# Kernel optimization log

Hardware: AMD Instinct MI355X
Metric: run time of the kernel (lower is better)

Reference implementation:

```python
import jax, jax.numpy as jnp
import numpy as np

N = 100000
C = 64
E = 3200000
NUM_LAYERS = 10
ALPHA = 0.9


def setup_inputs() -> dict:
    key = jax.random.key(0)
    k1, k2, k3, k4 = jax.random.split(key, 4)
    labels = jax.random.uniform(k1, (N, C), dtype=jnp.float32)
    mask = jax.random.randint(k2, (N,), 0, 2).astype(jnp.bool_)
    src = jax.random.randint(k3, (E,), 0, N, dtype=jnp.int32)
    dst = jax.random.randint(k4, (E,), 0, N, dtype=jnp.int32)
    return {"labels": labels, "mask": mask, "src": src, "dst": dst}


def reference(labels, mask, src, dst):
    # in-degrees: number of incoming edges per node, clamped to >= 1
    degs = jax.ops.segment_sum(jnp.ones((E,), dtype=jnp.float32), dst,
                               num_segments=N)
    degs = jnp.maximum(degs, 1.0)
    norm = (degs ** -0.5)[:, None]  # [N, 1]

    # seed only the masked (known) labels
    y = jnp.where(mask[:, None], labels, 0.0)
    last = (1.0 - ALPHA) * y

    def step(y, _):
        h = (y * norm)[src]                                   # gather  [E, C]
        agg = jax.ops.segment_sum(h, dst, num_segments=N)     # scatter [N, C]
        y = jnp.clip(last + ALPHA * agg * norm, 0.0, 1.0)     # post_step clamp
        return y, None

    y, _ = jax.lax.scan(step, y, None, length=NUM_LAYERS)
    return y
```

## Files before the change

### kernel.cpp

```cpp
#include <hip/hip_runtime.h>
#include <hip/hip_fp16.h>

#define N_LAYERS 10
#define ALPHA_F 0.9f
#define CAP 80
#define NRANGES 8

__global__ void detect_mask_kernel(const unsigned char* __restrict__ m,
                                   int* __restrict__ flag, int nbytes) {
    __shared__ int cnt;
    if (threadIdx.x == 0) cnt = 0;
    __syncthreads();
    int c = 0;
    for (int i = threadIdx.x; i < nbytes; i += blockDim.x) {
        if ((i & 3) != 0 && m[i] != 0) c++;
    }
    atomicAdd(&cnt, c);
    __syncthreads();
    if (threadIdx.x == 0) *flag = (cnt > 0) ? 1 : 0;
}

__global__ __launch_bounds__(256) void fillcap_kernel(
    const int* __restrict__ src, const int* __restrict__ dst,
    int* __restrict__ cnt, int* __restrict__ csr,
    int N, int E, int M, int range) {
    int r = blockIdx.x & (NRANGES - 1);
    int m = blockIdx.x >> 3;
    int rlo = r * range;
    int rhi = rlo + range; if (rhi > N) rhi = N;
    unsigned urlo = (unsigned)rlo;
    unsigned urng = (unsigned)(rhi - rlo);
    int stride = M * 256;
    int nv = E >> 2;
    const int4* s4p = (const int4*)src;
    const int4* d4p = (const int4*)dst;
    for (int i = m * 256 + threadIdx.x; i < nv; i += stride) {
        int4 d4 = d4p[i];
        int4 s4 = s4p[i];
        bool v0 = ((unsigned)d4.x - urlo) < urng;
        bool v1 = ((unsigned)d4.y - urlo) < urng;
        bool v2 = ((unsigned)d4.z - urlo) < urng;
        bool v3 = ((unsigned)d4.w - urlo) < urng;
        int p0 = v0 ? atomicAdd(cnt + d4.x, 1) : CAP;
        int p1 = v1 ? atomicAdd(cnt + d4.y, 1) : CAP;
        int p2 = v2 ? atomicAdd(cnt + d4.z, 1) : CAP;
        int p3 = v3 ? atomicAdd(cnt + d4.w, 1) : CAP;
        if (p0 < CAP) csr[(size_t)d4.x * CAP + p0] = s4.x;
        if (p1 < CAP) csr[(size_t)d4.y * CAP + p1] = s4.y;
        if (p2 < CAP) csr[(size_t)d4.z * CAP + p2] = s4.z;
        if (p3 < CAP) csr[(size_t)d4.w * CAP + p3] = s4.w;
    }
    if (m == 0) {
        for (int i = (nv << 2) + threadIdx.x; i < E; i += 256) {
            int d = dst[i];
            if (((unsigned)d - urlo) < urng) {
                int p = atomicAdd(cnt + d, 1);
                if (p < CAP) csr[(size_t)d * CAP + p] = src[i];
            }
        }
    }
}

__global__ void norm_kernel(const int* __restrict__ cnt,
                            float* __restrict__ norm, int N) {
    int i = blockIdx.x * blockDim.x + threadIdx.x;
    if (i < N) {
        int d = cnt[i];
        norm[i] = rsqrtf((float)(d > 0 ? d : 1));
    }
}

__global__ __launch_bounds__(256) void degree_kernel(
    const int* __restrict__ dst, int* __restrict__ cursor,
    int N, int E, int M, int range) {
    int r = blockIdx.x & (NRANGES - 1);
    int m = blockIdx.x >> 3;
    int rlo = r * range;
    int rhi = rlo + range; if (rhi > N) rhi = N;
    int stride = M * 256;
    for (int i = m * 256 + threadIdx.x; i < E; i += stride) {
        int d = dst[i];
        if (d >= rlo && d < rhi) atomicAdd(&cursor[d], 1);
    }
}

__global__ __launch_bounds__(256) void scan_blocks_kernel(
    const int* __restrict__ deg, int* __restrict__ local,
    int* __restrict__ btot, int N) {
    __shared__ int tmp[256];
    int i = blockIdx.x * 256 + threadIdx.x;
    int d = (i < N) ? deg[i] : 0;
    tmp[threadIdx.x] = d;
    __syncthreads();
    for (int off = 1; off < 256; off <<= 1) {
        int v = (threadIdx.x >= off) ? tmp[threadIdx.x - off] : 0;
        __syncthreads();
        tmp[threadIdx.x] += v;
        __syncthreads();
    }
    if (i < N) local[i] = tmp[threadIdx.x] - d;
    if (threadIdx.x == 255) btot[blockIdx.x] = tmp[255];
}

__global__ __launch_bounds__(512) void scan_tops_kernel(int* __restrict__ btot,
                                                        int nb) {
    __shared__ int tmp[512];
    int d = (threadIdx.x < nb) ? btot[threadIdx.x] : 0;
    tmp[threadIdx.x] = d;
    __syncthreads();
    for (int off = 1; off < 512; off <<= 1) {
        int v = (threadIdx.x >= off) ? tmp[threadIdx.x - off] : 0;
        __syncthreads();
        tmp[threadIdx.x] += v;
        __syncthreads();
    }
    if (threadIdx.x < nb) btot[threadIdx.x] = tmp[threadIdx.x] - d;
}

__global__ __launch_bounds__(256) void scan_apply_kernel(
    const int* __restrict__ local, const int* __restrict__ btot,
    int* __restrict__ cursor, int* __restrict__ offsets,
    float* __restrict__ norm, int N, int E) {
    int i = blockIdx.x * 256 + threadIdx.x;
    if (i >= N) return;
    int d = cursor[i];
    int off = local[i] + btot[blockIdx.x];
    offsets[i] = off;
    cursor[i] = off;
    norm[i] = rsqrtf((float)(d > 0 ? d : 1));
    if (i == N - 1) offsets[N] = E;
}

__global__ __launch_bounds__(256) void fill_kernel(
    const int* __restrict__ src, const int* __restrict__ dst,
    int* __restrict__ cursor, int* __restrict__ csr,
    int N, int E, int M, int range) {
    int r = blockIdx.x & (NRANGES - 1);
    int m = blockIdx.x >> 3;
    int rlo = r * range;
    int rhi = rlo + range; if (rhi > N) rhi = N;
    int stride = M * 256;
    for (int i = m * 256 + threadIdx.x; i < E; i += stride) {
        int d = dst[i];
        if (d >= rlo && d < rhi) {
            int pos = atomicAdd(&cursor[d], 1);
            csr[pos] = src[i];
        }
    }
}

__global__ void init_kernel(const float* __restrict__ labels,
                            const void* __restrict__ mask,
                            const int* __restrict__ flag,
                            const float* __restrict__ norm,
                            __half* __restrict__ y0,
                            __half* __restrict__ last_h, int NC) {
    int idx = blockIdx.x * blockDim.x + threadIdx.x;
    if (idx >= NC) return;
    int n = idx >> 6;
    bool m = (*flag) ? (((const unsigned char*)mask)[n] != 0)
                     : (((const int*)mask)[n] != 0);
    float ym = m ? labels[idx] : 0.0f;
    y0[idx] = __float2half(ym * norm[n]);
    last_h[idx] = __float2half(0.1f * ym);
}

__global__ __launch_bounds__(256) void prop_kernel(
    const int* __restrict__ degc, const int* __restrict__ offsets,
    const int* __restrict__ csr, const float* __restrict__ norm,
    const __half* __restrict__ last_h, const __half* __restrict__ yin,
    __half* __restrict__ yout, float* __restrict__ out_final,
    int N, int use_cap) {
    int wave = threadIdx.x >> 6;
    int lane = threadIdx.x & 63;
    int n = blockIdx.x * 4 + wave;
    if (n >= N) return;

    int deg; size_t base;
    if (use_cap) {
        deg = degc[n]; if (deg > CAP) deg = CAP;
        base = (size_t)n * CAP;
    } else {
        int s = offsets[n];
        deg = offsets[n + 1] - s;
        base = (size_t)s;
    }

    int grp = lane >> 3;
    int sub = lane & 7;
    const float4* yin4 = (const float4*)yin;

    float acc[8];
    #pragma unroll
    for (int k = 0; k < 8; ++k) acc[k] = 0.0f;

    for (int b0 = 0; b0 < deg; b0 += 64) {
        int cb = deg - b0; if (cb > 64) cb = 64;
        int li = lane < cb ? lane : cb - 1;
        int sid = csr[base + b0 + li];
        #pragma unroll
        for (int j = 0; j < 8; ++j) {
            int e = j * 8 + grp;
            int es = e < cb ? e : cb - 1;
            float msk = e < cb ? 1.0f : 0.0f;
            int s = __shfl(sid, es);
            float4 v = yin4[(size_t)s * 8 + sub];
            const __half2* h = (const __half2*)&v;
            float2 f0 = __half22float2(h[0]);
            float2 f1 = __half22float2(h[1]);
            float2 f2 = __half22float2(h[2]);
            float2 f3 = __half22float2(h[3]);
            acc[0] = fmaf(msk, f0.x, acc[0]);
            acc[1] = fmaf(msk, f0.y, acc[1]);
            acc[2] = fmaf(msk, f1.x, acc[2]);
            acc[3] = fmaf(msk, f1.y, acc[3]);
            acc[4] = fmaf(msk, f2.x, acc[4]);
            acc[5] = fmaf(msk, f2.y, acc[5]);
            acc[6] = fmaf(msk, f3.x, acc[6]);
            acc[7] = fmaf(msk, f3.y, acc[7]);
        }
    }

    #pragma unroll
    for (int k = 0; k < 8; ++k) {
        acc[k] += __shfl_xor(acc[k], 8);
        acc[k] += __shfl_xor(acc[k], 16);
        acc[k] += __shfl_xor(acc[k], 32);
    }

    float nrm = norm[n];
    float4 lv = ((const float4*)(last_h + ((size_t)n << 6)))[sub];
    const __half2* lh = (const __half2*)&lv;
    float2 g0 = __half22float2(lh[0]);
    float2 g1 = __half22float2(lh[1]);
    float2 g2 = __half22float2(lh[2]);
    float2 g3 = __half22float2(lh[3]);
    float lastv[8] = {g0.x, g0.y, g1.x, g1.y, g2.x, g2.y, g3.x, g3.y};

    float y[8];
    #pragma unroll
    for (int k = 0; k < 8; ++k) {
        float t = lastv[k] + ALPHA_F * acc[k] * nrm;
        y[k] = fminf(fmaxf(t, 0.0f), 1.0f);
    }

    if (grp == 0) {
        if (out_final) {
            float4* op = (float4*)(out_final + ((size_t)n << 6)) + (sub << 1);
            op[0] = make_float4(y[0], y[1], y[2], y[3]);
            op[1] = make_float4(y[4], y[5], y[6], y[7]);
        } else {
            __half2 h0 = __float22half2_rn(make_float2(y[0] * nrm, y[1] * nrm));
            __half2 h1 = __float22half2_rn(make_float2(y[2] * nrm, y[3] * nrm));
            __half2 h2 = __float22half2_rn(make_float2(y[4] * nrm, y[5] * nrm));
            __half2 h3 = __float22half2_rn(make_float2(y[6] * nrm, y[7] * nrm));
            float4 pack;
            ((__half2*)&pack)[0] = h0;
            ((__half2*)&pack)[1] = h1;
            ((__half2*)&pack)[2] = h2;
            ((__half2*)&pack)[3] = h3;
            ((float4*)(yout + ((size_t)n << 6)))[sub] = pack;
        }
    }
}

extern "C" void kernel_launch(void* const* d_in, const int* in_sizes, int n_in,
                              void* d_out, int out_size, void* d_ws,
                              size_t ws_size, hipStream_t stream) {
    const float* labels = (const float*)d_in[0];
    const void* mask = d_in[1];
    const int* src = (const int*)d_in[2];
    const int* dst = (const int*)d_in[3];
    int NC = in_sizes[0];
    int N = in_sizes[1];
    int E = in_sizes[2];

    char* p = (char*)d_ws;
    size_t used = 0;
    auto carve = [&](size_t bytes) -> char* {
        char* r = p;
        size_t a = (bytes + 255) & ~(size_t)255;
        p += a;
        used += a;
        return r;
    };
    int* flag      = (int*)carve(sizeof(int));
    float* norm    = (float*)carve((size_t)N * sizeof(float));
    int* cnt       = (int*)carve((size_t)(N + 1) * sizeof(int));
    __half* last_h = (__half*)carve((size_t)NC * sizeof(__half));
    __half* bufA   = (__half*)carve((size_t)NC * sizeof(__half));
    __half* bufB   = (__half*)carve((size_t)NC * sizeof(__half));

    size_t cap_need = ((size_t)N * CAP * sizeof(int) + 255) & ~(size_t)255;
    size_t cmp_need = (((size_t)E * sizeof(int) + 255) & ~(size_t)255) +
                      3 * (((size_t)(N + 1) * sizeof(int) + 255) & ~(size_t)255) +
                      1024 * sizeof(int) + 4096;
    bool use_cap = (used + cap_need) <= ws_size;

    int range = (N + NRANGES - 1) / NRANGES;
    int dbytes = N < 4096 ? N : 4096;
    detect_mask_kernel<<<1, 256, 0, stream>>>((const unsigned char*)mask, flag,
                                              dbytes);

    if (use_cap) {
        int* csr = (int*)carve((size_t)N * CAP * sizeof(int));
        hipMemsetAsync(cnt, 0, (size_t)N * sizeof(int), stream);
        int M = 256;
        fillcap_kernel<<<NRANGES * M, 256, 0, stream>>>(src, dst, cnt, csr, N,
                                                        E, M, range);
        norm_kernel<<<(N + 255) / 256, 256, 0, stream>>>(cnt, norm, N);
        init_kernel<<<(NC + 255) / 256, 256, 0, stream>>>(labels, mask, flag,
                                                          norm, bufA, last_h,
                                                          NC);
        __half* bufs[2] = {bufA, bufB};
        for (int l = 0; l < N_LAYERS; ++l) {
            bool fin = (l == N_LAYERS - 1);
            prop_kernel<<<(N + 3) / 4, 256, 0, stream>>>(
                cnt, cnt, csr, norm, last_h, bufs[l & 1], bufs[(l + 1) & 1],
                fin ? (float*)d_out : nullptr, N, 1);
        }
    } else {
        (void)cmp_need;
        int* offsets = (int*)carve((size_t)(N + 1) * sizeof(int));
        int* local   = (int*)carve((size_t)(N + 1) * sizeof(int));
        int* btot    = (int*)carve((size_t)1024 * sizeof(int));
        int* csr     = (int*)carve((size_t)E * sizeof(int));
        hipMemsetAsync(cnt, 0, (size_t)N * sizeof(int), stream);
        int M = 128;
        degree_kernel<<<NRANGES * M, 256, 0, stream>>>(dst, cnt, N, E, M,
                                                       range);
        int nscan = (N + 255) / 256;
        scan_blocks_kernel<<<nscan, 256, 0, stream>>>(cnt, local, btot, N);
        scan_tops_kernel<<<1, 512, 0, stream>>>(btot, nscan);
        scan_apply_kernel<<<nscan, 256, 0, stream>>>(local, btot, cnt, offsets,
                                                     norm, N, E);
        fill_kernel<<<NRANGES * M, 256, 0, stream>>>(src, dst, cnt, csr, N, E,
                                                     M, range);
        init_kernel<<<(NC + 255) / 256, 256, 0, stream>>>(labels, mask, flag,
                                                          norm, bufA, last_h,
                                                          NC);
        __half* bufs[2] = {bufA, bufB};
        for (int l = 0; l < N_LAYERS; ++l) {
            bool fin = (l == N_LAYERS - 1);
            prop_kernel<<<(N + 3) / 4, 256, 0, stream>>>(
                cnt, offsets, csr, norm, last_h, bufs[l & 1],
                bufs[(l + 1) & 1], fin ? (float*)d_out : nullptr, N, 0);
        }
    }
}
```

Measured before the change: 976.3 us.

## Split propagation into two channel-half passes with nontemporal loads and stores

Each layer's propagation now runs as two launches, each covering 32 of the 64 channels. Within a launch, 16 edge groups of 4 lanes gather 64-byte half rows, so the working set of gathered features per pass is halved and should fit better in cache. Nontemporal hints are added for the CSR index loads, the last_h loads and the output stores so they do not evict the gathered feature data. The cost is twice the launches and a second read of the CSR indices per layer.

```diff
diff --git a/kernel.cpp b/kernel.cpp
--- a/kernel.cpp
+++ b/kernel.cpp
@@ -5,6 +5,19 @@
 #define ALPHA_F 0.9f
 #define CAP 80
 #define NRANGES 8
+
+typedef float nfloat4 __attribute__((ext_vector_type(4)));
+
+__device__ __forceinline__ float4 nt_load4(const float4* p) {
+    nfloat4 v = __builtin_nontemporal_load((const nfloat4*)p);
+    float4 r;
+    r.x = v.x; r.y = v.y; r.z = v.z; r.w = v.w;
+    return r;
+}
+__device__ __forceinline__ void nt_store4(float4* p, float4 v) {
+    nfloat4 t = {v.x, v.y, v.z, v.w};
+    __builtin_nontemporal_store(t, (nfloat4*)p);
+}
 
 __global__ void detect_mask_kernel(const unsigned char* __restrict__ m,
                                    int* __restrict__ flag, int nbytes) {
@@ -170,7 +183,7 @@
     const int* __restrict__ csr, const float* __restrict__ norm,
     const __half* __restrict__ last_h, const __half* __restrict__ yin,
     __half* __restrict__ yout, float* __restrict__ out_final,
-    int N, int use_cap) {
+    int N, int use_cap, int half) {
     int wave = threadIdx.x >> 6;
     int lane = threadIdx.x & 63;
     int n = blockIdx.x * 4 + wave;
@@ -186,9 +199,10 @@
         base = (size_t)s;
     }
 
-    int grp = lane >> 3;
-    int sub = lane & 7;
+    int grp = lane >> 2;
+    int sub = lane & 3;
     const float4* yin4 = (const float4*)yin;
+    int hoff = half << 2;
 
     float acc[8];
     #pragma unroll
@@ -197,14 +211,14 @@
     for (int b0 = 0; b0 < deg; b0 += 64) {
         int cb = deg - b0; if (cb > 64) cb = 64;
         int li = lane < cb ? lane : cb - 1;
-        int sid = csr[base + b0 + li];
+        int sid = __builtin_nontemporal_load(csr + base + b0 + li);
         #pragma unroll
-        for (int j = 0; j < 8; ++j) {
-            int e = j * 8 + grp;
+        for (int j = 0; j < 4; ++j) {
+            int e = j * 16 + grp;
             int es = e < cb ? e : cb - 1;
             float msk = e < cb ? 1.0f : 0.0f;
             int s = __shfl(sid, es);
-            float4 v = yin4[(size_t)s * 8 + sub];
+            float4 v = yin4[(size_t)s * 8 + hoff + sub];
             const __half2* h = (const __half2*)&v;
             float2 f0 = __half22float2(h[0]);
             float2 f1 = __half22float2(h[1]);
@@ -223,13 +237,16 @@
 
     #pragma unroll
     for (int k = 0; k < 8; ++k) {
+        acc[k] += __shfl_xor(acc[k], 4);
         acc[k] += __shfl_xor(acc[k], 8);
         acc[k] += __shfl_xor(acc[k], 16);
         acc[k] += __shfl_xor(acc[k], 32);
     }
 
     float nrm = norm[n];
-    float4 lv = ((const float4*)(last_h + ((size_t)n << 6)))[sub];
+    const float4* lptr =
+        (const float4*)(last_h + ((size_t)n << 6) + (half << 5)) + sub;
+    float4 lv = nt_load4(lptr);
     const __half2* lh = (const __half2*)&lv;
     float2 g0 = __half22float2(lh[0]);
     float2 g1 = __half22float2(lh[1]);
@@ -246,9 +263,10 @@
 
     if (grp == 0) {
         if (out_final) {
-            float4* op = (float4*)(out_final + ((size_t)n << 6)) + (sub << 1);
-            op[0] = make_float4(y[0], y[1], y[2], y[3]);
-            op[1] = make_float4(y[4], y[5], y[6], y[7]);
+            float4* op = (float4*)(out_final + ((size_t)n << 6) + (half << 5)) +
+                         (sub << 1);
+            nt_store4(op, make_float4(y[0], y[1], y[2], y[3]));
+            nt_store4(op + 1, make_float4(y[4], y[5], y[6], y[7]));
         } else {
             __half2 h0 = __float22half2_rn(make_float2(y[0] * nrm, y[1] * nrm));
             __half2 h1 = __float22half2_rn(make_float2(y[2] * nrm, y[3] * nrm));
@@ -259,7 +277,9 @@
             ((__half2*)&pack)[1] = h1;
             ((__half2*)&pack)[2] = h2;
             ((__half2*)&pack)[3] = h3;
-            ((float4*)(yout + ((size_t)n << 6)))[sub] = pack;
+            float4* op =
+                (float4*)(yout + ((size_t)n << 6) + (half << 5)) + sub;
+            nt_store4(op, pack);
         }
     }
 }
@@ -292,9 +312,6 @@
     __half* bufB   = (__half*)carve((size_t)NC * sizeof(__half));
 
     size_t cap_need = ((size_t)N * CAP * sizeof(int) + 255) & ~(size_t)255;
-    size_t cmp_need = (((size_t)E * sizeof(int) + 255) & ~(size_t)255) +
-                      3 * (((size_t)(N + 1) * sizeof(int) + 255) & ~(size_t)255) +
-                      1024 * sizeof(int) + 4096;
     bool use_cap = (used + cap_need) <= ws_size;
 
     int range = (N + NRANGES - 1) / NRANGES;
@@ -315,12 +332,13 @@
         __half* bufs[2] = {bufA, bufB};
         for (int l = 0; l < N_LAYERS; ++l) {
             bool fin = (l == N_LAYERS - 1);
-            prop_kernel<<<(N + 3) / 4, 256, 0, stream>>>(
-                cnt, cnt, csr, norm, last_h, bufs[l & 1], bufs[(l + 1) & 1],
-                fin ? (float*)d_out : nullptr, N, 1);
+            for (int h = 0; h < 2; ++h) {
+                prop_kernel<<<(N + 3) / 4, 256, 0, stream>>>(
+                    cnt, cnt, csr, norm, last_h, bufs[l & 1], bufs[(l + 1) & 1],
+                    fin ? (float*)d_out : nullptr, N, 1, h);
+            }
         }
     } else {
-        (void)cmp_need;
         int* offsets = (int*)carve((size_t)(N + 1) * sizeof(int));
         int* local   = (int*)carve((size_t)(N + 1) * sizeof(int));
         int* btot    = (int*)carve((size_t)1024 * sizeof(int));
@@ -342,9 +360,11 @@
         __half* bufs[2] = {bufA, bufB};
         for (int l = 0; l < N_LAYERS; ++l) {
             bool fin = (l == N_LAYERS - 1);
-            prop_kernel<<<(N + 3) / 4, 256, 0, stream>>>(
-                cnt, offsets, csr, norm, last_h, bufs[l & 1],
-                bufs[(l + 1) & 1], fin ? (float*)d_out : nullptr, N, 0);
-        }
-    }
-}
+            for (int h = 0; h < 2; ++h) {
+                prop_kernel<<<(N + 3) / 4, 256, 0, stream>>>(
+                    cnt, offsets, csr, norm, last_h, bufs[l & 1],
+                    bufs[(l + 1) & 1], fin ? (float*)d_out : nullptr, N, 0, h);
+            }
+        }
+    }
+}
```

After: 1.315 ms. 1.35x slower.
